# Performance work log

Measured on AMD Instinct MI355X. Metric: run time of the kernel, lower is better.

## Reference

```python
import jax, jax.numpy as jnp
import numpy as np

B, S, N, D, T = 128, 128, 196, 512, 12


def setup_inputs() -> dict:
    key = jax.random.key(0)
    ks = jax.random.split(key, 20)
    nrm = lambda i, shape, s: jax.random.normal(ks[i], shape, jnp.float32) * s
    w = lambda i, shape: nrm(i, shape, 1.0 / np.sqrt(shape[-1]))
    return {
        "ctx": nrm(0, (B, S, D), 1.0),
        "q": nrm(1, (B, 2 * D), 1.0),
        "k": nrm(2, (B, D, N), 1.0),
        "mem0": nrm(3, (1, D), 0.02),
        "ctrl0": nrm(4, (1, D), 0.02),
        # ControlUnit params
        "Wp": w(5, (T, D, 2 * D)), "bp": jnp.zeros((T, D), jnp.float32),
        "Wcq": w(6, (D, 2 * D)), "bcq": jnp.zeros((D,), jnp.float32),
        "Wca": w(7, (1, D)), "bca": jnp.zeros((1,), jnp.float32),
        # ReadUnit params
        "Wrm": w(8, (D, D)), "brm": jnp.zeros((D,), jnp.float32),
        "Wrc": w(9, (D, 2 * D)), "brc": jnp.zeros((D,), jnp.float32),
        "Wra": w(10, (1, D)), "bra": jnp.zeros((1,), jnp.float32),
        # WriteUnit params
        "Wwc": w(11, (D, 2 * D)), "bwc": jnp.zeros((D,), jnp.float32),
    }


def reference(ctx, q, k, mem0, ctrl0, Wp, bp, Wcq, bcq, Wca, bca,
              Wrm, brm, Wrc, brc, Wra, bra, Wwc, bwc):
    b = q.shape[0]
    c = jnp.broadcast_to(ctrl0, (b, D))
    m = jnp.broadcast_to(mem0, (b, D))
    for t in range(T):
        # --- control unit (alpha_entmax with alpha=1.0 == softmax) ---
        p = q @ Wp[t].T + bp[t]                                # [B, D]
        cc = jnp.concatenate([c, p], axis=1) @ Wcq.T + bcq     # [B, D]
        ctx_p = cc[:, None, :] * ctx                           # [B, S, D]
        aw = jax.nn.softmax(ctx_p @ Wca.T + bca, axis=1)       # [B, S, 1]
        c = (aw * ctx).sum(axis=1)                             # [B, D]
        # --- read unit ---
        mm = (m @ Wrm.T + brm)[:, :, None]                     # [B, D, 1]
        kc = jnp.concatenate([mm * k, k], axis=1)              # [B, 2D, N]
        rc = kc.transpose(0, 2, 1) @ Wrc.T + brc               # [B, N, D]
        logit = ((rc * c[:, None, :]) @ Wra.T + bra)[..., 0]   # [B, N]
        rw = jax.nn.softmax(logit, axis=1)[:, None, :]         # [B, 1, N]
        r = (rw * k).sum(axis=2)                               # [B, D]
        # --- write unit (no self-attention / memory gate) ---
        m = jnp.concatenate([r, m], axis=1) @ Wwc.T + bwc      # [B, D]
    return m
```

## Files before the change

kernel.cpp:

```cpp
#include <hip/hip_runtime.h>
#include <hip/hip_bf16.h>
#include <cstdint>

#define D  512
#define D2 1024
#define BB 128
#define SS 128
#define NN 196
#define TT 12

typedef unsigned short u16;
typedef __attribute__((ext_vector_type(8))) short short8v;
typedef __attribute__((ext_vector_type(4))) float f32x4;

__device__ __forceinline__ float bf2f(u16 h){
  union { unsigned int u; float f; } v; v.u = ((unsigned int)h) << 16; return v.f;
}

__device__ __forceinline__ float LDX(const void* p, size_t i, int isbf){
  if (isbf) return bf2f(((const u16*)p)[i]);
  return ((const float*)p)[i];
}

__device__ __forceinline__ float4 LD4(const void* p, size_t i, int isbf){
  if (isbf){
    ushort4 w = *(const ushort4*)((const u16*)p + i);
    return make_float4(bf2f(w.x), bf2f(w.y), bf2f(w.z), bf2f(w.w));
  }
  return *(const float4*)((const float*)p + i);
}

__device__ __forceinline__ void bfsplit(float x, short &h, short &l){
  unsigned u = __float_as_uint(x);
  unsigned hu = u & 0xFFFF0000u;
  float r = x - __uint_as_float(hu);
  h = (short)(u >> 16);
  l = (short)(__float_as_uint(r) >> 16);
}

__global__ __launch_bounds__(256) void k_detect(const u16* ctx, int* flag){
  __shared__ int cnt;
  if (threadIdx.x == 0) cnt = 0;
  __syncthreads();
  int bad = 0;
  for (int i = threadIdx.x; i < 8192; i += 256){
    int e = (ctx[i] >> 7) & 0xFF;
    if (e == 0xFF || (e != 0 && (e < 90 || e > 160))) bad++;
  }
  atomicAdd(&cnt, bad);
  __syncthreads();
  if (threadIdx.x == 0) *flag = (cnt > 100) ? 0 : 1;
}

__global__ __launch_bounds__(256) void k_prep1(const void* Wcq, const void* Wca,
      const void* Wwc, const void* Wrm, const void* Wrc, const void* Wra,
      const void* bp, const void* bcq, const void* ctrl0, const void* mem0, const void* brm,
      float* W1f, float* Wwcf, float* WrmTf, float* W2f,
      float* P, float* pp2, float* ubase, float* mmb, const int* flag){
  const int isbf = *flag;
  __shared__ float lds[32][33];
  int bk = blockIdx.x, tid = threadIdx.x;
  int tx = tid & 31, ty = tid >> 5;
  if (bk >= 1216){
    int ib = bk - 1216;
    int lane = tid & 63, w = tid >> 6;
    int grp = lane >> 3, k = lane & 7;
    int isU = (ib < 16);
    int o = (isU ? ib : ib - 16)*32 + w*8 + grp;
    const void* vec = isU ? ctrl0 : mem0;
    const void* mat = isU ? Wcq : Wrm;
    int ld = isU ? D2 : D;
    float acc = 0.f;
    #pragma unroll 4
    for (int it = 0; it < 16; it++){
      int d = it*32 + k*4;
      float4 v = LD4(vec, d, isbf);
      float4 m = LD4(mat, (size_t)o*ld + d, isbf);
      acc += v.x*m.x + v.y*m.y + v.z*m.z + v.w*m.w;
    }
    acc += __shfl_xor(acc, 1, 64);
    acc += __shfl_xor(acc, 2, 64);
    acc += __shfl_xor(acc, 4, 64);
    if (k == 0){
      if (isU) ubase[o] = acc * LDX(Wca, o, isbf);
      else     mmb[o]   = acc + LDX(brm, o, isbf);
    }
    return;
  }
  if (bk >= 1152){
    int l = bk - 1152;
    for (int idx = l*256 + tid; idx < 786432; idx += 64*256){
      int j = (idx >> 7) & 511;
      pp2[idx] = LDX(bcq, j, isbf) * LDX(Wca, j, isbf);
    }
    return;
  }
  if (bk >= 1088){
    int l = bk - 1088;
    for (int idx = l*256 + tid; idx < 786432; idx += 64*256)
      P[idx] = LDX(bp, idx >> 7, isbf);
    return;
  }
  if (bk >= 1024){
    int l = bk - 1024;
    if (isbf){
      const u16* w = (const u16*)Wrc; const u16* s = (const u16*)Wra;
      for (int idx = l*256 + tid; idx < 524288; idx += 64*256)
        W2f[idx] = bf2f(w[idx]) * bf2f(s[idx >> 10]);
    } else {
      const float* w = (const float*)Wrc; const float* s = (const float*)Wra;
      for (int idx = l*256 + tid; idx < 524288; idx += 64*256)
        W2f[idx] = w[idx] * s[idx >> 10];
    }
    return;
  }
  const void* in = nullptr; const void* scale = nullptr; float* out = nullptr;
  int ld = 0, R = 0, tR = 0, tC = 0;
  if (bk < 256)      { int l = bk;       in = Wcq; ld = 1024; R = 512; out = W1f;  scale = Wca; tR = l & 15; tC = l >> 4; }
  else if (bk < 768) { int l = bk - 256; in = Wwc; ld = 1024; R = 512; out = Wwcf; tR = l & 15; tC = l >> 4; }
  else               { int l = bk - 768; in = Wrm; ld = 512;  R = 512; out = WrmTf;tR = l & 15; tC = l >> 4; }
  int r0 = tR*32, c0 = tC*32;
  #pragma unroll
  for (int kk = 0; kk < 4; kk++){
    int r = r0 + ty + kk*8;
    float v = LDX(in, (size_t)r*ld + c0 + tx, isbf);
    if (scale) v *= LDX(scale, r, isbf);
    lds[tx][ty + kk*8] = v;
  }
  __syncthreads();
  #pragma unroll
  for (int kk = 0; kk < 4; kk++){
    int oc = ty + kk*8;
    out[(size_t)(c0 + oc)*R + r0 + tx] = lds[oc][tx];
  }
}

__global__ __launch_bounds__(256) void k_pack(const void* q, u16* QF,
                                              const void* kmat, float* kT, const int* flag){
  const int isbf = *flag;
  __shared__ float lds[64][201];
  int bk = blockIdx.x, tid = threadIdx.x;
  if (bk < 128){
    u16* QH = QF;
    u16* QL = QF + 131072;
    for (int idx = bk*256 + tid; idx < 131072; idx += 128*256){
      int b = idx >> 10, x = idx & 1023;
      int o = ((x >> 3) << 10) + (b << 3) + (x & 7);
      if (isbf){
        QH[o] = ((const u16*)q)[idx];
        QL[o] = 0;
      } else {
        short h, l;
        bfsplit(((const float*)q)[idx], h, l);
        QH[o] = (u16)h;
        QL[o] = (u16)l;
      }
    }
    return;
  }
  int l = bk - 128;
  int b = l >> 3, dt = l & 7;
  int d0 = dt*64;
  int r = tid >> 2, q4 = tid & 3;
  const size_t rowbase = ((size_t)b*D + d0 + r)*NN;
  #pragma unroll
  for (int p = 0; p < 13; p++){
    int j = q4 + p*4;
    if (j < 49){
      float4 v = LD4(kmat, rowbase + 4*j, isbf);
      *(float4*)&lds[r][4*j] = v;
    }
  }
  __syncthreads();
  int n_loc = tid >> 4, f = tid & 15;
  #pragma unroll
  for (int p = 0; p < 13; p++){
    int n = p*16 + n_loc;
    if (n < NN){
      float4 v = make_float4(lds[4*f][n], lds[4*f+1][n], lds[4*f+2][n], lds[4*f+3][n]);
      *(float4*)&kT[((size_t)b*NN + n)*D + d0 + 4*f] = v;
    }
  }
}

__global__ __launch_bounds__(256) void k_Pmfma(const void* Wp, const u16* QF,
                                               float* P, const int* flag){
  const int isbf = *flag;
  const u16* QH = QF;
  const u16* QL = QF + 131072;
  int bk = blockIdx.x;
  int mt = bk >> 2, kc = bk & 3;
  int m0 = mt * 32;
  int tid = threadIdx.x;
  int ln = tid & 63, w = tid >> 6;
  int msub = w >> 1, nh = w & 1;
  int row  = m0 + msub*16 + (ln & 15);
  int koff = ln >> 4;
  f32x4 acc[4];
  #pragma unroll
  for (int i = 0; i < 4; i++) acc[i] = (f32x4){0.f, 0.f, 0.f, 0.f};

  for (int ks = 0; ks < 8; ks++){
    int k0 = kc*256 + ks*32;
    short8v ah, al;
    if (isbf){
      const u16* wr = (const u16*)Wp + (size_t)row*D2 + k0 + koff*8;
      ah = *(const short8v*)wr;
    } else {
      const float* wr = (const float*)Wp + (size_t)row*D2 + k0 + koff*8;
      float4 f0 = *(const float4*)wr;
      float4 f1 = *(const float4*)(wr + 4);
      float fs[8] = {f0.x, f0.y, f0.z, f0.w, f1.x, f1.y, f1.z, f1.w};
      #pragma unroll
      for (int j = 0; j < 8; j++){
        short h, l;
        bfsplit(fs[j], h, l);
        ah[j] = h; al[j] = l;
      }
    }
    int qrow = ((k0 >> 3) + koff) << 10;
    #pragma unroll
    for (int nt = 0; nt < 4; nt++){
      int col = (nh*4 + nt)*16 + (ln & 15);
      short8v bh = *(const short8v*)(QH + qrow + (col << 3));
      acc[nt] = __builtin_amdgcn_mfma_f32_16x16x32_bf16(ah, bh, acc[nt], 0, 0, 0);
      if (!isbf){
        short8v bl = *(const short8v*)(QL + qrow + (col << 3));
        acc[nt] = __builtin_amdgcn_mfma_f32_16x16x32_bf16(ah, bl, acc[nt], 0, 0, 0);
        acc[nt] = __builtin_amdgcn_mfma_f32_16x16x32_bf16(al, bh, acc[nt], 0, 0, 0);
      }
    }
  }
  int orow = m0 + msub*16 + (ln >> 4)*4;
  #pragma unroll
  for (int nt = 0; nt < 4; nt++){
    int b = (nh*4 + nt)*16 + (ln & 15);
    #pragma unroll
    for (int r = 0; r < 4; r++)
      atomicAdd(&P[(size_t)(orow + r)*BB + b], acc[nt][r]);
  }
}

__global__ __launch_bounds__(512) void k_pp2(const float* P, const void* Wcq,
                                             const void* Wca, float* pp2, const int* flag){
  const int isbf = *flag;
  int bk = blockIdx.x;
  int t = bk >> 6; int r = bk & 63; int jt = r >> 1; int kc = r & 1;
  int tid = threadIdx.x;
  int b = tid & 127;
  int ih = __builtin_amdgcn_readfirstlane(tid >> 7);
  int j0 = jt*16 + ih*4;
  float acc[4] = {0.f, 0.f, 0.f, 0.f};
  int e0k = kc*256;
  if (isbf){
    const u16* w = (const u16*)Wcq;
    for (int e = e0k; e < e0k + 256; e += 8){
      float a[8];
      #pragma unroll
      for (int u = 0; u < 8; u++) a[u] = P[(size_t)(t*D + e + u)*BB + b];
      #pragma unroll
      for (int kk = 0; kk < 4; kk++){
        ushort4 w0 = *(const ushort4*)(w + (size_t)(j0+kk)*D2 + D + e);
        ushort4 w1 = *(const ushort4*)(w + (size_t)(j0+kk)*D2 + D + e + 4);
        acc[kk] += a[0]*bf2f(w0.x) + a[1]*bf2f(w0.y) + a[2]*bf2f(w0.z) + a[3]*bf2f(w0.w)
                 + a[4]*bf2f(w1.x) + a[5]*bf2f(w1.y) + a[6]*bf2f(w1.z) + a[7]*bf2f(w1.w);
      }
    }
  } else {
    const float* w = (const float*)Wcq;
    for (int e = e0k; e < e0k + 256; e += 8){
      float a[8];
      #pragma unroll
      for (int u = 0; u < 8; u++) a[u] = P[(size_t)(t*D + e + u)*BB + b];
      #pragma unroll
      for (int kk = 0; kk < 4; kk++){
        float4 w0 = *(const float4*)(w + (size_t)(j0+kk)*D2 + D + e);
        float4 w1 = *(const float4*)(w + (size_t)(j0+kk)*D2 + D + e + 4);
        acc[kk] += a[0]*w0.x + a[1]*w0.y + a[2]*w0.z + a[3]*w0.w
                 + a[4]*w1.x + a[5]*w1.y + a[6]*w1.z + a[7]*w1.w;
      }
    }
  }
  #pragma unroll
  for (int kk = 0; kk < 4; kk++)
    atomicAdd(&pp2[(size_t)(t*D + j0 + kk)*BB + b], acc[kk] * LDX(Wca, j0 + kk, isbf));
}

__global__ __launch_bounds__(256) void k_initB(const float* ubase, const void* mem0,
                                               const float* pp2,
                                               float* u0, float* act0, const int* flag){
  const int isbf = *flag;
  for (int idx = blockIdx.x*256 + threadIdx.x; idx < 2*D*BB; idx += 64*256){
    if (idx < D*BB) u0[idx] = ubase[idx >> 7] + pp2[idx];
    else          { int x = idx - D*BB; act0[D*BB + x] = LDX(mem0, x >> 7, isbf); }
  }
}

__global__ __launch_bounds__(512) void k_K1(const void* ctx, const float* u_cur,
                                            float* gbuf, const float* pbuf, const float* kT,
                                            float* r_out, int t, const int* flag){
  __shared__ float sm[1024];
  int bk = blockIdx.x, tid = threadIdx.x;
  const int isbf = *flag;
  if (bk < 512){
    if (t == 0) return;
    float* lg   = sm;
    float* red  = sm + 256;
    float* psum = sm + 512;
    int b = bk & 127, qc = bk >> 7;
    if (tid < 256){
      float s;
      if (tid < NN){
        s = 0.f;
        #pragma unroll
        for (int c = 0; c < 8; c++)
          s += pbuf[((size_t)c*BB + b)*256 + tid];
      } else s = -INFINITY;
      lg[tid] = s; red[tid] = s;
    }
    __syncthreads();
    for (int off = 128; off; off >>= 1){ if (tid < off) red[tid] = fmaxf(red[tid], red[tid+off]); __syncthreads(); }
    float M = red[0];
    __syncthreads();
    if (tid < 256){ float e = (tid < NN) ? __expf(lg[tid] - M) : 0.f; lg[tid] = e; red[tid] = e; }
    __syncthreads();
    for (int off = 128; off; off >>= 1){ if (tid < off) red[tid] += red[tid+off]; __syncthreads(); }
    float inv = 1.f / red[0];
    int ng = tid >> 7, dl = tid & 127;
    const float* kTb = kT + ((size_t)b*NN + ng*49)*D + qc*128 + dl;
    float acc = 0.f;
    for (int j = 0; j < 49; j++)
      acc += lg[ng*49 + j] * kTb[(size_t)j*D];
    psum[ng*128 + dl] = acc;
    __syncthreads();
    if (tid < 128)
      r_out[(size_t)(qc*128 + tid)*BB + b] =
        (psum[tid] + psum[128 + tid] + psum[256 + tid] + psum[384 + tid]) * inv;
    return;
  }
  if (t >= TT) return;
  int l = bk - 512;
  int b = l & 127, sc = l >> 7;
  float* us = sm;
  us[tid] = u_cur[(size_t)tid*BB + b];
  __syncthreads();
  int lane = tid & 63, wv = tid >> 6;
  float ur[8];
  #pragma unroll
  for (int j = 0; j < 8; j++) ur[j] = us[lane*8 + j];
  #pragma unroll
  for (int rr = 0; rr < 4; rr++){
    int s = sc*32 + wv*4 + rr;
    size_t base = ((size_t)(b*SS + s))*D + lane*8;
    float4 c0 = LD4(ctx, base, isbf);
    float4 c1 = LD4(ctx, base + 4, isbf);
    float dot = ur[0]*c0.x + ur[1]*c0.y + ur[2]*c0.z + ur[3]*c0.w
              + ur[4]*c1.x + ur[5]*c1.y + ur[6]*c1.z + ur[7]*c1.w;
    #pragma unroll
    for (int off = 32; off; off >>= 1) dot += __shfl_down(dot, off, 64);
    if (lane == 0) gbuf[b*SS + s] = dot;
  }
}

__global__ __launch_bounds__(512) void k_K2(const void* ctx, const float* gbuf, float* cbuf,
                                            const float* act_prev, float* act_cur,
                                            float* u_nxt, const float* pp2_next,
                                            const float* Wwcf, int t, const int* flag){
  __shared__ float sm[768];
  int bk = blockIdx.x, tid = threadIdx.x;
  const int isbf = *flag;
  if (bk < 512){
    float* lg   = sm;
    float* red  = sm + 128;
    float* psum = sm + 256;
    int b = bk & 127, qc = bk >> 7;
    if (tid < 128){ float v = gbuf[b*SS + tid]; lg[tid] = v; red[tid] = v; }
    __syncthreads();
    for (int off = 64; off; off >>= 1){ if (tid < off) red[tid] = fmaxf(red[tid], red[tid+off]); __syncthreads(); }
    float M = red[0];
    __syncthreads();
    if (tid < 128){ float e = __expf(lg[tid] - M); lg[tid] = e; red[tid] = e; }
    __syncthreads();
    for (int off = 64; off; off >>= 1){ if (tid < off) red[tid] += red[tid+off]; __syncthreads(); }
    float inv = 1.f / red[0];
    int sg = tid >> 7, dl = tid & 127;
    int d = qc*128 + dl;
    float acc = 0.f;
    for (int j = 0; j < 32; j++){
      int s = sg*32 + j;
      acc += lg[s] * LDX(ctx, ((size_t)(b*SS + s))*D + d, isbf);
    }
    psum[sg*128 + dl] = acc;
    __syncthreads();
    if (tid < 128)
      cbuf[(size_t)(qc*128 + tid)*BB + b] =
        (psum[tid] + psum[128 + tid] + psum[256 + tid] + psum[384 + tid]) * inv;
    return;
  }
  int b = tid & 127;
  int ih = __builtin_amdgcn_readfirstlane(tid >> 7);
  if (bk < 1024){
    if (t == 0) return;
    int l = bk - 512;
    int it = l >> 3, kc = l & 7;
    int ih0 = ih & 1, ih1 = ih >> 1;
    int i0 = it*8 + ih0*4;
    int e0 = kc*128 + ih1*64;
    float acc[4] = {0.f,0.f,0.f,0.f};
    for (int e = e0; e < e0 + 64; e += 8){
      float av[8];
      #pragma unroll
      for (int u = 0; u < 8; u++) av[u] = act_prev[(size_t)(e+u)*BB + b];
      #pragma unroll
      for (int u = 0; u < 8; u++){
        float4 w0 = *(const float4*)(Wwcf + (size_t)(e+u)*D + i0);
        acc[0]+=av[u]*w0.x; acc[1]+=av[u]*w0.y; acc[2]+=av[u]*w0.z; acc[3]+=av[u]*w0.w;
      }
    }
    #pragma unroll
    for (int kk = 0; kk < 4; kk++)
      atomicAdd(&act_cur[(size_t)(D + i0 + kk)*BB + b], acc[kk]);
  } else {
    if (t >= TT-1) return;
    int l = bk - 1024;
    for (int x = l*512 + tid; x < D*BB; x += 32*512) u_nxt[x] = pp2_next[x];
  }
}

__global__ __launch_bounds__(512) void k_KC1(const void* kmat, const float* cbuf,
                                             const float* act_cur, const float* W2f,
                                             const float* WrmTf, const void* brm,
                                             const float* mmb, float* pbuf,
                                             const float* W1f, float* u_nxt,
                                             float* act_nxt, const void* bwc,
                                             int t, const int* flag){
  __shared__ float cb[512];
  __shared__ float mv[512];
  __shared__ float wv2[256];
  __shared__ float mmv[128];
  __shared__ float u2[128];
  int bk = blockIdx.x, tid = threadIdx.x;
  const int isbf = *flag;
  if (bk < 512){
    int b = bk & 127, ch2 = bk >> 7;
    int d0 = ch2*128;
    cb[tid] = cbuf[(size_t)tid*BB + b];
    if (t > 0) mv[tid] = act_cur[(size_t)(D + tid)*BB + b];
    __syncthreads();
    if (tid < 256){
      int e = (tid < 128) ? (d0 + tid) : (D + d0 + (tid - 128));
      float c0=0.f,c1=0.f,c2=0.f,c3=0.f,c4=0.f,c5=0.f,c6=0.f,c7=0.f;
      for (int j = 0; j < 512; j += 8){
        c0 += cb[j  ]*W2f[(size_t)(j  )*D2 + e];
        c1 += cb[j+1]*W2f[(size_t)(j+1)*D2 + e];
        c2 += cb[j+2]*W2f[(size_t)(j+2)*D2 + e];
        c3 += cb[j+3]*W2f[(size_t)(j+3)*D2 + e];
        c4 += cb[j+4]*W2f[(size_t)(j+4)*D2 + e];
        c5 += cb[j+5]*W2f[(size_t)(j+5)*D2 + e];
        c6 += cb[j+6]*W2f[(size_t)(j+6)*D2 + e];
        c7 += cb[j+7]*W2f[(size_t)(j+7)*D2 + e];
      }
      wv2[tid] = (((c0+c1)+(c2+c3)) + ((c4+c5)+(c6+c7)));
    } else if (tid < 384){
      int tm = tid - 256;
      int d = d0 + tm;
      if (t == 0){
        mmv[tm] = mmb[d];
      } else {
        float c0=0.f,c1=0.f,c2=0.f,c3=0.f,c4=0.f,c5=0.f,c6=0.f,c7=0.f;
        for (int j = 0; j < 512; j += 8){
          c0 += mv[j  ]*WrmTf[(size_t)(j  )*D + d];
          c1 += mv[j+1]*WrmTf[(size_t)(j+1)*D + d];
          c2 += mv[j+2]*WrmTf[(size_t)(j+2)*D + d];
          c3 += mv[j+3]*WrmTf[(size_t)(j+3)*D + d];
          c4 += mv[j+4]*WrmTf[(size_t)(j+4)*D + d];
          c5 += mv[j+5]*WrmTf[(size_t)(j+5)*D + d];
          c6 += mv[j+6]*WrmTf[(size_t)(j+6)*D + d];
          c7 += mv[j+7]*WrmTf[(size_t)(j+7)*D + d];
        }
        mmv[tm] = LDX(brm, d, isbf) + (((c0+c1)+(c2+c3)) + ((c4+c5)+(c6+c7)));
      }
    }
    __syncthreads();
    if (tid < 128) u2[tid] = wv2[tid]*mmv[tid] + wv2[128 + tid];
    __syncthreads();
    int half = tid >> 8;
    int n = tid & 255;
    int dd0 = half*64;
    float part = 0.f;
    if (n < NN){
      float c[8];
      #pragma unroll
      for (int u = 0; u < 8; u++) c[u] = 0.f;
      if (isbf){
        const u16* kb = (const u16*)kmat + (size_t)b*D*NN + (size_t)(d0+dd0)*NN + n;
        for (int dd = 0; dd < 64; dd += 8){
          #pragma unroll
          for (int u = 0; u < 8; u++) c[u] += u2[dd0+dd+u]*bf2f(kb[(size_t)(dd+u)*NN]);
        }
      } else {
        const float* kb = (const float*)kmat + (size_t)b*D*NN + (size_t)(d0+dd0)*NN + n;
        for (int dd = 0; dd < 64; dd += 8){
          #pragma unroll
          for (int u = 0; u < 8; u++) c[u] += u2[dd0+dd+u]*kb[(size_t)(dd+u)*NN];
        }
      }
      part = (((c[0]+c[1]) + (c[2]+c[3])) + ((c[4]+c[5]) + (c[6]+c[7])));
    }
    int chunk = ch2*2 + half;
    pbuf[((size_t)chunk*BB + b)*256 + n] = part;
    return;
  }
  int b = tid & 127;
  int ih = __builtin_amdgcn_readfirstlane(tid >> 7);
  if (bk < 768){
    if (t >= TT-1) return;
    int l = bk - 512;
    int jt = l >> 1, kc = l & 1;
    int j = jt*4 + ih;
    float c0 = 0.f, c1 = 0.f, c2 = 0.f, c3 = 0.f, c4 = 0.f, c5 = 0.f, c6 = 0.f, c7 = 0.f;
    int e0 = kc*256;
    for (int e = e0; e < e0 + 256; e += 8){
      c0 += cbuf[(e  )*BB + b] * W1f[(size_t)(e  )*D + j];
      c1 += cbuf[(e+1)*BB + b] * W1f[(size_t)(e+1)*D + j];
      c2 += cbuf[(e+2)*BB + b] * W1f[(size_t)(e+2)*D + j];
      c3 += cbuf[(e+3)*BB + b] * W1f[(size_t)(e+3)*D + j];
      c4 += cbuf[(e+4)*BB + b] * W1f[(size_t)(e+4)*D + j];
      c5 += cbuf[(e+5)*BB + b] * W1f[(size_t)(e+5)*D + j];
      c6 += cbuf[(e+6)*BB + b] * W1f[(size_t)(e+6)*D + j];
      c7 += cbuf[(e+7)*BB + b] * W1f[(size_t)(e+7)*D + j];
    }
    float acc = (((c0+c1)+(c2+c3)) + ((c4+c5)+(c6+c7)));
    atomicAdd(&u_nxt[(size_t)j*BB + b], acc);
  } else {
    int l = bk - 768;
    for (int x = l*512 + tid; x < D*BB; x += 32*512)
      act_nxt[D*BB + x] = LDX(bwc, x >> 7, isbf);
  }
}

__global__ __launch_bounds__(512) void k_moutA(const float* act_fin, const float* Wwcf,
                                               float* act_out){
  int bk = blockIdx.x, tid = threadIdx.x;
  int b = tid & 127;
  int ih = __builtin_amdgcn_readfirstlane(tid >> 7);
  int it = bk >> 3, kc = bk & 7;
  int ih0 = ih & 1, ih1 = ih >> 1;
  int i0 = it*8 + ih0*4;
  int e0 = kc*128 + ih1*64;
  float acc[4] = {0.f,0.f,0.f,0.f};
  for (int e = e0; e < e0 + 64; e += 8){
    float av[8];
    #pragma unroll
    for (int u = 0; u < 8; u++) av[u] = act_fin[(size_t)(e+u)*BB + b];
    #pragma unroll
    for (int u = 0; u < 8; u++){
      float4 w0 = *(const float4*)(Wwcf + (size_t)(e+u)*D + i0);
      acc[0]+=av[u]*w0.x; acc[1]+=av[u]*w0.y; acc[2]+=av[u]*w0.z; acc[3]+=av[u]*w0.w;
    }
  }
  #pragma unroll
  for (int kk = 0; kk < 4; kk++)
    atomicAdd(&act_out[(size_t)(D + i0 + kk)*BB + b], acc[kk]);
}

__global__ __launch_bounds__(256) void k_outT(const float* act_fin, void* out, const int* flag){
  const int isbf = *flag;
  __shared__ float lds[32][33];
  int bk = blockIdx.x;
  int it = bk >> 2, bt = bk & 3;
  int tx = threadIdx.x & 31, ty = threadIdx.x >> 5;
  #pragma unroll
  for (int kk = 0; kk < 4; kk++){
    int i = it*32 + ty + kk*8;
    lds[tx][ty + kk*8] = act_fin[(size_t)(D + i)*BB + bt*32 + tx];
  }
  __syncthreads();
  if (isbf){
    __hip_bfloat16* o = (__hip_bfloat16*)out;
    #pragma unroll
    for (int kk = 0; kk < 4; kk++){
      int bb = bt*32 + ty + kk*8;
      o[(size_t)bb*D + it*32 + tx] = __float2bfloat16(lds[ty + kk*8][tx]);
    }
  } else {
    float* o = (float*)out;
    #pragma unroll
    for (int kk = 0; kk < 4; kk++){
      int bb = bt*32 + ty + kk*8;
      o[(size_t)bb*D + it*32 + tx] = lds[ty + kk*8][tx];
    }
  }
}

extern "C" void kernel_launch(void* const* d_in, const int* in_sizes, int n_in,
                              void* d_out, int out_size, void* d_ws, size_t ws_size,
                              hipStream_t stream){
  const void* ctx  = d_in[0];
  const void* q    = d_in[1];
  const void* kmat = d_in[2];
  const void* mem0 = d_in[3];
  const void* ctrl0= d_in[4];
  const void* Wp   = d_in[5];
  const void* bp   = d_in[6];
  const void* Wcq  = d_in[7];
  const void* bcq  = d_in[8];
  const void* Wca  = d_in[9];
  const void* Wrm  = d_in[11];
  const void* brm  = d_in[12];
  const void* Wrc  = d_in[13];
  const void* Wra  = d_in[15];
  const void* Wwc  = d_in[17];
  const void* bwc  = d_in[18];

  float* W      = (float*)d_ws;
  float* qT     = W;
  float* P      = W + 131072;
  float* pp2    = W + 917504;
  float* W1f    = W + 1703936;
  float* W2f    = W + 1966080;
  float* Wwcf   = W + 2490368;
  float* WrmTf  = W + 3014656;
  float* cbuf   = W + 3276800;
  float* actb   = W + 3538944;
  float* ubuf   = W + 3801088;
  int*   flag   = (int*)(W + 3932160);
  float* ubase  = W + 3932224;
  float* mmb    = W + 3932736;
  float* gbuf   = W + 3933248;
  float* pbuf   = P;
  float* kT     = W + 4194304;

  hipLaunchKernelGGL(k_detect, dim3(1), dim3(256), 0, stream, (const u16*)ctx, flag);
  hipLaunchKernelGGL(k_prep1, dim3(1248), dim3(256), 0, stream,
                     Wcq, Wca, Wwc, Wrm, Wrc, Wra, bp, bcq, ctrl0, mem0, brm,
                     W1f, Wwcf, WrmTf, W2f, P, pp2, ubase, mmb, flag);
  hipLaunchKernelGGL(k_pack, dim3(1152), dim3(256), 0, stream,
                     q, (u16*)qT, kmat, kT, flag);
  hipLaunchKernelGGL(k_Pmfma, dim3(768), dim3(256), 0, stream, Wp, (const u16*)qT, P, flag);
  hipLaunchKernelGGL(k_pp2,  dim3(768), dim3(512), 0, stream, P, Wcq, Wca, pp2, flag);
  hipLaunchKernelGGL(k_initB, dim3(64), dim3(256), 0, stream,
                     ubase, mem0, pp2, ubuf, actb, flag);

  for (int t = 0; t < TT; t++){
    int cur = t & 1, nxt = 1 - cur;
    float* act_cur  = actb + cur*131072;
    float* act_prev = actb + nxt*131072;
    hipLaunchKernelGGL(k_K1, dim3(1024), dim3(512), 0, stream,
                       ctx, ubuf + cur*65536, gbuf, pbuf, kT,
                       act_prev, t, flag);
    hipLaunchKernelGGL(k_K2, dim3(1056), dim3(512), 0, stream,
                       ctx, gbuf, cbuf, act_prev, act_cur,
                       ubuf + nxt*65536,
                       pp2 + ((t+1 < TT) ? (t+1)*65536 : 0), Wwcf, t, flag);
    hipLaunchKernelGGL(k_KC1, dim3(800), dim3(512), 0, stream,
                       kmat, cbuf, act_cur, W2f, WrmTf, brm, mmb, pbuf,
                       W1f, ubuf + nxt*65536,
                       actb + nxt*131072, bwc, t, flag);
  }
  hipLaunchKernelGGL(k_K1, dim3(512), dim3(512), 0, stream,
                     ctx, ubuf, gbuf, pbuf, kT,
                     actb + 131072, TT, flag);
  hipLaunchKernelGGL(k_moutA, dim3(512), dim3(512), 0, stream,
                     actb + 131072, Wwcf, actb);
  hipLaunchKernelGGL(k_outT, dim3(64), dim3(256), 0, stream, actb, d_out, flag);
}
```

Before: 1.010 ms.

## Fold Wrm into Wwc to merge per-step kernels from three to two

Precomputes GF = Wwc·Wrm (and a bias mmc = Wrm·bwc + brm) so the read unit's memory projection comes straight from the previous step's [r, m] activation. The next memory state no longer has to be formed before mm. This removes a serial dependency, so the ctx logit pass and the control softmax merge into one kernel. The step loop now launches two kernels per iteration instead of three. In exchange the mm matvec runs over 1024 inputs instead of 512, there is an extra precompute kernel, and the float summation order changes.

```diff
diff --git a/kernel.cpp b/kernel.cpp
--- a/kernel.cpp
+++ b/kernel.cpp
@@ -55,8 +55,9 @@
 __global__ __launch_bounds__(256) void k_prep1(const void* Wcq, const void* Wca,
       const void* Wwc, const void* Wrm, const void* Wrc, const void* Wra,
       const void* bp, const void* bcq, const void* ctrl0, const void* mem0, const void* brm,
+      const void* bwc,
       float* W1f, float* Wwcf, float* WrmTf, float* W2f,
-      float* P, float* pp2, float* ubase, float* mmb, const int* flag){
+      float* P, float* pp2, float* ubase, float* mmb, float* mmc, const int* flag){
   const int isbf = *flag;
   __shared__ float lds[32][33];
   int bk = blockIdx.x, tid = threadIdx.x;
@@ -65,11 +66,11 @@
     int ib = bk - 1216;
     int lane = tid & 63, w = tid >> 6;
     int grp = lane >> 3, k = lane & 7;
-    int isU = (ib < 16);
-    int o = (isU ? ib : ib - 16)*32 + w*8 + grp;
-    const void* vec = isU ? ctrl0 : mem0;
-    const void* mat = isU ? Wcq : Wrm;
-    int ld = isU ? D2 : D;
+    int kind = ib >> 4;
+    int o = (ib & 15)*32 + w*8 + grp;
+    const void* vec = (kind == 0) ? ctrl0 : ((kind == 1) ? mem0 : bwc);
+    const void* mat = (kind == 0) ? Wcq : Wrm;
+    int ld = (kind == 0) ? D2 : D;
     float acc = 0.f;
     #pragma unroll 4
     for (int it = 0; it < 16; it++){
@@ -82,8 +83,9 @@
     acc += __shfl_xor(acc, 2, 64);
     acc += __shfl_xor(acc, 4, 64);
     if (k == 0){
-      if (isU) ubase[o] = acc * LDX(Wca, o, isbf);
-      else     mmb[o]   = acc + LDX(brm, o, isbf);
+      if (kind == 0)      ubase[o] = acc * LDX(Wca, o, isbf);
+      else if (kind == 1) mmb[o]   = acc + LDX(brm, o, isbf);
+      else                mmc[o]   = acc + LDX(brm, o, isbf);
     }
     return;
   }
@@ -132,6 +134,26 @@
   for (int kk = 0; kk < 4; kk++){
     int oc = ty + kk*8;
     out[(size_t)(c0 + oc)*R + r0 + tx] = lds[oc][tx];
+  }
+}
+
+__global__ __launch_bounds__(256) void k_gf(const float* Wwcf, const float* WrmTf, float* GF){
+  __shared__ float wr[4][512];
+  int o0 = blockIdx.x * 4, tid = threadIdx.x;
+  for (int idx = tid; idx < 4*512; idx += 256)
+    wr[idx >> 9][idx & 511] = Wwcf[(size_t)(o0 + (idx >> 9))*D + (idx & 511)];
+  __syncthreads();
+  float a0[4] = {0.f,0.f,0.f,0.f}, a1[4] = {0.f,0.f,0.f,0.f};
+  for (int j = 0; j < 512; j++){
+    float x = WrmTf[(size_t)j*D + tid];
+    float y = WrmTf[(size_t)j*D + 256 + tid];
+    #pragma unroll
+    for (int r = 0; r < 4; r++){ a0[r] += wr[r][j]*x; a1[r] += wr[r][j]*y; }
+  }
+  #pragma unroll
+  for (int r = 0; r < 4; r++){
+    GF[(size_t)(o0 + r)*D + tid]       = a0[r];
+    GF[(size_t)(o0 + r)*D + 256 + tid] = a1[r];
   }
 }
 
@@ -296,10 +318,13 @@
   }
 }
 
-__global__ __launch_bounds__(512) void k_K1(const void* ctx, const float* u_cur,
-                                            float* gbuf, const float* pbuf, const float* kT,
-                                            float* r_out, int t, const int* flag){
-  __shared__ float sm[1024];
+__global__ __launch_bounds__(512) void k_KA(const void* ctx, const float* u_cur,
+                                            const float* pbuf, const float* kT,
+                                            float* r_out, float* cbuf,
+                                            float* u_nxt, const float* pp2_next,
+                                            float* act_cur, const void* bwc,
+                                            int t, const int* flag){
+  __shared__ float sm[1280];
   int bk = blockIdx.x, tid = threadIdx.x;
   const int isbf = *flag;
   if (bk < 512){
@@ -338,43 +363,33 @@
         (psum[tid] + psum[128 + tid] + psum[256 + tid] + psum[384 + tid]) * inv;
     return;
   }
-  if (t >= TT) return;
-  int l = bk - 512;
-  int b = l & 127, sc = l >> 7;
-  float* us = sm;
-  us[tid] = u_cur[(size_t)tid*BB + b];
-  __syncthreads();
-  int lane = tid & 63, wv = tid >> 6;
-  float ur[8];
-  #pragma unroll
-  for (int j = 0; j < 8; j++) ur[j] = us[lane*8 + j];
-  #pragma unroll
-  for (int rr = 0; rr < 4; rr++){
-    int s = sc*32 + wv*4 + rr;
-    size_t base = ((size_t)(b*SS + s))*D + lane*8;
-    float4 c0 = LD4(ctx, base, isbf);
-    float4 c1 = LD4(ctx, base + 4, isbf);
-    float dot = ur[0]*c0.x + ur[1]*c0.y + ur[2]*c0.z + ur[3]*c0.w
-              + ur[4]*c1.x + ur[5]*c1.y + ur[6]*c1.z + ur[7]*c1.w;
-    #pragma unroll
-    for (int off = 32; off; off >>= 1) dot += __shfl_down(dot, off, 64);
-    if (lane == 0) gbuf[b*SS + s] = dot;
-  }
-}
-
-__global__ __launch_bounds__(512) void k_K2(const void* ctx, const float* gbuf, float* cbuf,
-                                            const float* act_prev, float* act_cur,
-                                            float* u_nxt, const float* pp2_next,
-                                            const float* Wwcf, int t, const int* flag){
-  __shared__ float sm[768];
-  int bk = blockIdx.x, tid = threadIdx.x;
-  const int isbf = *flag;
-  if (bk < 512){
-    float* lg   = sm;
-    float* red  = sm + 128;
-    float* psum = sm + 256;
-    int b = bk & 127, qc = bk >> 7;
-    if (tid < 128){ float v = gbuf[b*SS + tid]; lg[tid] = v; red[tid] = v; }
+  if (bk < 1024){
+    if (t >= TT) return;
+    int l = bk - 512;
+    int b = l & 127, qc = l >> 7;
+    float* us   = sm;
+    float* lg   = sm + 512;
+    float* red  = sm + 640;
+    float* psum = sm + 768;
+    us[tid] = u_cur[(size_t)tid*BB + b];
+    __syncthreads();
+    int lane = tid & 63, wv = tid >> 6;
+    float ur[8];
+    #pragma unroll
+    for (int j = 0; j < 8; j++) ur[j] = us[lane*8 + j];
+    for (int rr = 0; rr < 16; rr++){
+      int s = wv*16 + rr;
+      size_t base = ((size_t)(b*SS + s))*D + lane*8;
+      float4 c0 = LD4(ctx, base, isbf);
+      float4 c1 = LD4(ctx, base + 4, isbf);
+      float dot = ur[0]*c0.x + ur[1]*c0.y + ur[2]*c0.z + ur[3]*c0.w
+                + ur[4]*c1.x + ur[5]*c1.y + ur[6]*c1.z + ur[7]*c1.w;
+      #pragma unroll
+      for (int off = 32; off; off >>= 1) dot += __shfl_down(dot, off, 64);
+      if (lane == 0) lg[s] = dot;
+    }
+    __syncthreads();
+    if (tid < 128) red[tid] = lg[tid];
     __syncthreads();
     for (int off = 64; off; off >>= 1){ if (tid < off) red[tid] = fmaxf(red[tid], red[tid+off]); __syncthreads(); }
     float M = red[0];
@@ -397,45 +412,27 @@
         (psum[tid] + psum[128 + tid] + psum[256 + tid] + psum[384 + tid]) * inv;
     return;
   }
-  int b = tid & 127;
-  int ih = __builtin_amdgcn_readfirstlane(tid >> 7);
-  if (bk < 1024){
-    if (t == 0) return;
-    int l = bk - 512;
-    int it = l >> 3, kc = l & 7;
-    int ih0 = ih & 1, ih1 = ih >> 1;
-    int i0 = it*8 + ih0*4;
-    int e0 = kc*128 + ih1*64;
-    float acc[4] = {0.f,0.f,0.f,0.f};
-    for (int e = e0; e < e0 + 64; e += 8){
-      float av[8];
-      #pragma unroll
-      for (int u = 0; u < 8; u++) av[u] = act_prev[(size_t)(e+u)*BB + b];
-      #pragma unroll
-      for (int u = 0; u < 8; u++){
-        float4 w0 = *(const float4*)(Wwcf + (size_t)(e+u)*D + i0);
-        acc[0]+=av[u]*w0.x; acc[1]+=av[u]*w0.y; acc[2]+=av[u]*w0.z; acc[3]+=av[u]*w0.w;
-      }
-    }
-    #pragma unroll
-    for (int kk = 0; kk < 4; kk++)
-      atomicAdd(&act_cur[(size_t)(D + i0 + kk)*BB + b], acc[kk]);
-  } else {
+  if (bk < 1056){
     if (t >= TT-1) return;
     int l = bk - 1024;
     for (int x = l*512 + tid; x < D*BB; x += 32*512) u_nxt[x] = pp2_next[x];
-  }
-}
-
-__global__ __launch_bounds__(512) void k_KC1(const void* kmat, const float* cbuf,
-                                             const float* act_cur, const float* W2f,
-                                             const float* WrmTf, const void* brm,
-                                             const float* mmb, float* pbuf,
-                                             const float* W1f, float* u_nxt,
-                                             float* act_nxt, const void* bwc,
-                                             int t, const int* flag){
+  } else {
+    if (t == 0) return;
+    int l = bk - 1056;
+    for (int x = l*512 + tid; x < D*BB; x += 32*512)
+      act_cur[D*BB + x] = LDX(bwc, x >> 7, isbf);
+  }
+}
+
+__global__ __launch_bounds__(512) void k_KC(const void* kmat, const float* cbuf,
+                                            const float* act_prev, const float* W2f,
+                                            const float* GF, const float* mmc,
+                                            const float* mmb, const float* Wwcf,
+                                            float* act_cur, float* pbuf,
+                                            const float* W1f, float* u_nxt,
+                                            int t, const int* flag){
   __shared__ float cb[512];
-  __shared__ float mv[512];
+  __shared__ float ap[1024];
   __shared__ float wv2[256];
   __shared__ float mmv[128];
   __shared__ float u2[128];
@@ -445,7 +442,10 @@
     int b = bk & 127, ch2 = bk >> 7;
     int d0 = ch2*128;
     cb[tid] = cbuf[(size_t)tid*BB + b];
-    if (t > 0) mv[tid] = act_cur[(size_t)(D + tid)*BB + b];
+    if (t > 0){
+      ap[tid]       = act_prev[(size_t)tid*BB + b];
+      ap[512 + tid] = act_prev[(size_t)(512 + tid)*BB + b];
+    }
     __syncthreads();
     if (tid < 256){
       int e = (tid < 128) ? (d0 + tid) : (D + d0 + (tid - 128));
@@ -468,17 +468,17 @@
         mmv[tm] = mmb[d];
       } else {
         float c0=0.f,c1=0.f,c2=0.f,c3=0.f,c4=0.f,c5=0.f,c6=0.f,c7=0.f;
-        for (int j = 0; j < 512; j += 8){
-          c0 += mv[j  ]*WrmTf[(size_t)(j  )*D + d];
-          c1 += mv[j+1]*WrmTf[(size_t)(j+1)*D + d];
-          c2 += mv[j+2]*WrmTf[(size_t)(j+2)*D + d];
-          c3 += mv[j+3]*WrmTf[(size_t)(j+3)*D + d];
-          c4 += mv[j+4]*WrmTf[(size_t)(j+4)*D + d];
-          c5 += mv[j+5]*WrmTf[(size_t)(j+5)*D + d];
-          c6 += mv[j+6]*WrmTf[(size_t)(j+6)*D + d];
-          c7 += mv[j+7]*WrmTf[(size_t)(j+7)*D + d];
+        for (int j = 0; j < 1024; j += 8){
+          c0 += ap[j  ]*GF[(size_t)(j  )*D + d];
+          c1 += ap[j+1]*GF[(size_t)(j+1)*D + d];
+          c2 += ap[j+2]*GF[(size_t)(j+2)*D + d];
+          c3 += ap[j+3]*GF[(size_t)(j+3)*D + d];
+          c4 += ap[j+4]*GF[(size_t)(j+4)*D + d];
+          c5 += ap[j+5]*GF[(size_t)(j+5)*D + d];
+          c6 += ap[j+6]*GF[(size_t)(j+6)*D + d];
+          c7 += ap[j+7]*GF[(size_t)(j+7)*D + d];
         }
-        mmv[tm] = LDX(brm, d, isbf) + (((c0+c1)+(c2+c3)) + ((c4+c5)+(c6+c7)));
+        mmv[tm] = mmc[d] + (((c0+c1)+(c2+c3)) + ((c4+c5)+(c6+c7)));
       }
     }
     __syncthreads();
@@ -513,9 +513,30 @@
   }
   int b = tid & 127;
   int ih = __builtin_amdgcn_readfirstlane(tid >> 7);
-  if (bk < 768){
+  if (bk < 1024){
+    if (t == 0) return;
+    int l = bk - 512;
+    int it = l >> 3, kc = l & 7;
+    int ih0 = ih & 1, ih1 = ih >> 1;
+    int i0 = it*8 + ih0*4;
+    int e0 = kc*128 + ih1*64;
+    float acc[4] = {0.f,0.f,0.f,0.f};
+    for (int e = e0; e < e0 + 64; e += 8){
+      float av[8];
+      #pragma unroll
+      for (int u = 0; u < 8; u++) av[u] = act_prev[(size_t)(e+u)*BB + b];
+      #pragma unroll
+      for (int u = 0; u < 8; u++){
+        float4 w0 = *(const float4*)(Wwcf + (size_t)(e+u)*D + i0);
+        acc[0]+=av[u]*w0.x; acc[1]+=av[u]*w0.y; acc[2]+=av[u]*w0.z; acc[3]+=av[u]*w0.w;
+      }
+    }
+    #pragma unroll
+    for (int kk = 0; kk < 4; kk++)
+      atomicAdd(&act_cur[(size_t)(D + i0 + kk)*BB + b], acc[kk]);
+  } else {
     if (t >= TT-1) return;
-    int l = bk - 512;
+    int l = bk - 1024;
     int jt = l >> 1, kc = l & 1;
     int j = jt*4 + ih;
     float c0 = 0.f, c1 = 0.f, c2 = 0.f, c3 = 0.f, c4 = 0.f, c5 = 0.f, c6 = 0.f, c7 = 0.f;
@@ -532,10 +553,6 @@
     }
     float acc = (((c0+c1)+(c2+c3)) + ((c4+c5)+(c6+c7)));
     atomicAdd(&u_nxt[(size_t)j*BB + b], acc);
-  } else {
-    int l = bk - 768;
-    for (int x = l*512 + tid; x < D*BB; x += 32*512)
-      act_nxt[D*BB + x] = LDX(bwc, x >> 7, isbf);
   }
 }
 
@@ -627,17 +644,19 @@
   int*   flag   = (int*)(W + 3932160);
   float* ubase  = W + 3932224;
   float* mmb    = W + 3932736;
-  float* gbuf   = W + 3933248;
+  float* mmc    = W + 3933248;
   float* pbuf   = P;
   float* kT     = W + 4194304;
+  float* GF     = W + 17039360;
 
   hipLaunchKernelGGL(k_detect, dim3(1), dim3(256), 0, stream, (const u16*)ctx, flag);
-  hipLaunchKernelGGL(k_prep1, dim3(1248), dim3(256), 0, stream,
-                     Wcq, Wca, Wwc, Wrm, Wrc, Wra, bp, bcq, ctrl0, mem0, brm,
-                     W1f, Wwcf, WrmTf, W2f, P, pp2, ubase, mmb, flag);
+  hipLaunchKernelGGL(k_prep1, dim3(1264), dim3(256), 0, stream,
+                     Wcq, Wca, Wwc, Wrm, Wrc, Wra, bp, bcq, ctrl0, mem0, brm, bwc,
+                     W1f, Wwcf, WrmTf, W2f, P, pp2, ubase, mmb, mmc, flag);
   hipLaunchKernelGGL(k_pack, dim3(1152), dim3(256), 0, stream,
                      q, (u16*)qT, kmat, kT, flag);
   hipLaunchKernelGGL(k_Pmfma, dim3(768), dim3(256), 0, stream, Wp, (const u16*)qT, P, flag);
+  hipLaunchKernelGGL(k_gf, dim3(256), dim3(256), 0, stream, Wwcf, WrmTf, GF);
   hipLaunchKernelGGL(k_pp2,  dim3(768), dim3(512), 0, stream, P, Wcq, Wca, pp2, flag);
   hipLaunchKernelGGL(k_initB, dim3(64), dim3(256), 0, stream,
                      ubase, mem0, pp2, ubuf, actb, flag);
@@ -646,21 +665,19 @@
     int cur = t & 1, nxt = 1 - cur;
     float* act_cur  = actb + cur*131072;
     float* act_prev = actb + nxt*131072;
-    hipLaunchKernelGGL(k_K1, dim3(1024), dim3(512), 0, stream,
-                       ctx, ubuf + cur*65536, gbuf, pbuf, kT,
-                       act_prev, t, flag);
-    hipLaunchKernelGGL(k_K2, dim3(1056), dim3(512), 0, stream,
-                       ctx, gbuf, cbuf, act_prev, act_cur,
-                       ubuf + nxt*65536,
-                       pp2 + ((t+1 < TT) ? (t+1)*65536 : 0), Wwcf, t, flag);
-    hipLaunchKernelGGL(k_KC1, dim3(800), dim3(512), 0, stream,
-                       kmat, cbuf, act_cur, W2f, WrmTf, brm, mmb, pbuf,
-                       W1f, ubuf + nxt*65536,
-                       actb + nxt*131072, bwc, t, flag);
-  }
-  hipLaunchKernelGGL(k_K1, dim3(512), dim3(512), 0, stream,
-                     ctx, ubuf, gbuf, pbuf, kT,
-                     actb + 131072, TT, flag);
+    hipLaunchKernelGGL(k_KA, dim3(1088), dim3(512), 0, stream,
+                       ctx, ubuf + cur*65536, pbuf, kT,
+                       act_prev, cbuf, ubuf + nxt*65536,
+                       pp2 + ((t+1 < TT) ? (t+1)*65536 : 0),
+                       act_cur, bwc, t, flag);
+    hipLaunchKernelGGL(k_KC, dim3(1280), dim3(512), 0, stream,
+                       kmat, cbuf, act_prev, W2f, GF, mmc, mmb, Wwcf,
+                       act_cur, pbuf, W1f, ubuf + nxt*65536, t, flag);
+  }
+  hipLaunchKernelGGL(k_KA, dim3(1088), dim3(512), 0, stream,
+                     ctx, ubuf, pbuf, kT,
+                     actb + 131072, cbuf, ubuf, pp2,
+                     actb, bwc, TT, flag);
   hipLaunchKernelGGL(k_moutA, dim3(512), dim3(512), 0, stream,
                      actb + 131072, Wwcf, actb);
   hipLaunchKernelGGL(k_outT, dim3(64), dim3(256), 0, stream, actb, d_out, flag);
```

New measurement: 1.314 ms. 1.3x slower.
